# Kernel tuning notes

Measured on AMD Instinct MI355X. Metric: run time of the kernel, lower is better.

## Reference

```python
import jax, jax.numpy as jnp
import numpy as np

N_HEAD = 16
POSE = 5
YAW = 1
END_X, END_Y = 18, 32
THETA = 1000.0
LN_EPS = 1e-5

def compute_axial_cis(dim, end_x, end_y, theta):
    # Axial 2D rotary: dim is per-head dim; dim//4 freqs per spatial axis.
    n = dim // 4
    freqs = 1.0 / (theta ** (jnp.arange(0, dim, 4)[:n].astype(jnp.float32) / dim))
    t = jnp.arange(end_x * end_y, dtype=jnp.float32)
    t_x = t % end_x
    t_y = jnp.floor(t / end_x)
    ang = jnp.concatenate([t_x[:, None] * freqs[None, :], t_y[:, None] * freqs[None, :]], axis=-1)  # [L, dim//2]
    return jnp.cos(ang), jnp.sin(ang)

def apply_rotary(x, cos, sin):
    # x: [B,H,L,D]; complex pairing = consecutive (even, odd) lanes, as in view_as_complex
    xe, xo = x[..., 0::2], x[..., 1::2]
    oe = xe * cos - xo * sin
    oo = xe * sin + xo * cos
    return jnp.stack([oe, oo], axis=-1).reshape(x.shape)

def layernorm(z, g, b):
    m = jnp.mean(z, axis=-1, keepdims=True)
    v = jnp.mean(jnp.square(z - m), axis=-1, keepdims=True)
    return (z - m) * jax.lax.rsqrt(v + LN_EPS) * g + b

def setup_inputs() -> dict:
    key = jax.random.key(0)
    ks = jax.random.split(key, 8)
    B, T, C = 16, 582, 1024
    x = jax.random.normal(ks[0], (B, T, C), dtype=jnp.float32)
    # additive causal mask (0 keep / -1e9 masked), as a float attn_mask
    causal = jnp.tril(jnp.ones((T, T), dtype=jnp.float32))
    attn_mask = jnp.broadcast_to(jnp.where(causal > 0, 0.0, -1e9), (B, T, T))
    s = 0.02
    Wq = jax.random.normal(ks[1], (C, C), dtype=jnp.float32) * s
    Wk = jax.random.normal(ks[2], (C, C), dtype=jnp.float32) * s
    Wv = jax.random.normal(ks[3], (C, C), dtype=jnp.float32) * s
    Wo = jax.random.normal(ks[4], (C, C), dtype=jnp.float32) * s
    q_ln_g = jnp.ones((C,), jnp.float32); q_ln_b = jnp.zeros((C,), jnp.float32)
    k_ln_g = jnp.ones((C,), jnp.float32); k_ln_b = jnp.zeros((C,), jnp.float32)
    return {"x": x, "attn_mask": attn_mask, "Wq": Wq, "Wk": Wk, "Wv": Wv, "Wo": Wo,
            "q_ln_g": q_ln_g, "q_ln_b": q_ln_b, "k_ln_g": k_ln_g, "k_ln_b": k_ln_b}

def reference(x, attn_mask, Wq, Wk, Wv, Wo, q_ln_g, q_ln_b, k_ln_g, k_ln_b):
    B, T, C = x.shape
    H = N_HEAD
    D = C // H
    q = layernorm(x @ Wq.T, q_ln_g, q_ln_b)
    k = layernorm(x @ Wk.T, k_ln_g, k_ln_b)
    v = (x @ Wv.T).reshape(B, T, H, D).transpose(0, 2, 1, 3)
    q = q.reshape(B, T, H, D).transpose(0, 2, 1, 3)
    k = k.reshape(B, T, H, D).transpose(0, 2, 1, 3)
    prefix = POSE + YAW
    if T > prefix:  # static shape condition
        cos, sin = compute_axial_cis(D, END_X, END_Y, THETA)
        L = T - prefix
        cos, sin = cos[:L], sin[:L]  # [L, D//2]
        q = jnp.concatenate([q[:, :, :prefix], apply_rotary(q[:, :, prefix:], cos, sin)], axis=2)
        k = jnp.concatenate([k[:, :, :prefix], apply_rotary(k[:, :, prefix:], cos, sin)], axis=2)
    scale = 1.0 / jnp.sqrt(jnp.float32(D))
    scores = jnp.einsum("bhqd,bhkd->bhqk", q, k) * scale + attn_mask[:, None, :, :]
    att = jax.nn.softmax(scores, axis=-1)
    y = jnp.einsum("bhqk,bhkd->bhqd", att, v)
    y = y.transpose(0, 2, 1, 3).reshape(B, T, C)
    return y @ Wo.T
```

## Files before the change

kernel.cpp:

```cpp
#include <hip/hip_runtime.h>
#include <hip/hip_bf16.h>

typedef short bf16x8 __attribute__((ext_vector_type(8)));
typedef short bf16x4 __attribute__((ext_vector_type(4)));
typedef float f32x4  __attribute__((ext_vector_type(4)));

#define LDP 72

__device__ __forceinline__ float bits2f(short u) {
  return __uint_as_float(((unsigned int)(unsigned short)u) << 16);
}
__device__ __forceinline__ short f2bits(float f) {
  __hip_bfloat16 h = __float2bfloat16(f);
  return *reinterpret_cast<short*>(&h);
}
__device__ __forceinline__ void gld16(const short* g, short* l) {
  __builtin_amdgcn_global_load_lds(
      (const __attribute__((address_space(1))) void*)g,
      (__attribute__((address_space(3))) void*)l, 16, 0, 0);
}

__global__ __launch_bounds__(256)
void cvt_x_kernel(const float* __restrict__ src, short* __restrict__ dst, long n) {
  long i = ((long)blockIdx.x * 256 + threadIdx.x) * 4;
  if (i + 3 < n) {
    float4 v = *(const float4*)(src + i);
    bf16x4 o;
    o[0] = f2bits(v.x); o[1] = f2bits(v.y); o[2] = f2bits(v.z); o[3] = f2bits(v.w);
    *(bf16x4*)(dst + i) = o;
  }
}

__global__ __launch_bounds__(256)
void cvt_w_kernel(const float* __restrict__ w0, const float* __restrict__ w1,
                  const float* __restrict__ w2, const float* __restrict__ w3,
                  short* __restrict__ dst) {
  long i = ((long)blockIdx.x * 256 + threadIdx.x) * 4;
  int sel = (int)(i >> 20);
  const float* s = (sel == 0) ? w0 : (sel == 1) ? w1 : (sel == 2) ? w2 : w3;
  long off = i & ((1L << 20) - 1);
  float4 v = *(const float4*)(s + off);
  bf16x4 o;
  o[0] = f2bits(v.x); o[1] = f2bits(v.y); o[2] = f2bits(v.z); o[3] = f2bits(v.w);
  *(bf16x4*)(dst + i) = o;
}

template<int MODE>
__global__ __launch_bounds__(256)
void gemm_nt(const short* __restrict__ A, const short* __restrict__ Bm,
             float* __restrict__ OutF, short* __restrict__ Oq,
             short* __restrict__ Ok, short* __restrict__ Ov,
             int M, int K, int N, int T, int TPAD) {
  __shared__ short As[128 * 32];
  __shared__ short Bs[128 * 32];
  const int tid = threadIdx.x;
  const int w = tid >> 6, l = tid & 63;
  const int wr = w >> 1, wc = w & 1;
  const int lg = l >> 4, lo = l & 15;
  const long row0 = (long)blockIdx.x * 128;
  const long col0 = (long)blockIdx.y * 128;

  const int c2 = w * 2;
  const int lrow = l >> 2, lcol = (l & 3) * 8;
  long ga0 = row0 + c2 * 16 + lrow;      if (ga0 > M - 1) ga0 = M - 1;
  long ga1 = row0 + c2 * 16 + 16 + lrow; if (ga1 > M - 1) ga1 = M - 1;
  long gb0 = col0 + c2 * 16 + lrow;
  long gb1 = gb0 + 16;
  const short* pa0 = &A[ga0 * K + lcol];
  const short* pa1 = &A[ga1 * K + lcol];
  const short* pb0 = &Bm[gb0 * K + lcol];
  const short* pb1 = &Bm[gb1 * K + lcol];
  short* la0 = &As[c2 * 512];
  short* la1 = &As[c2 * 512 + 512];
  short* lb0 = &Bs[c2 * 512];
  short* lb1 = &Bs[c2 * 512 + 512];

  f32x4 acc[4][4] = {};

  for (int kt = 0; kt < K; kt += 32) {
    __syncthreads();
    gld16(pa0 + kt, la0);
    gld16(pa1 + kt, la1);
    gld16(pb0 + kt, lb0);
    gld16(pb1 + kt, lb1);
    __syncthreads();
    bf16x8 af[4], bfr[4];
#pragma unroll
    for (int mi = 0; mi < 4; ++mi)
      af[mi] = *(const bf16x8*)(&As[(wr * 64 + mi * 16 + lo) * 32 + lg * 8]);
#pragma unroll
    for (int ni = 0; ni < 4; ++ni)
      bfr[ni] = *(const bf16x8*)(&Bs[(wc * 64 + ni * 16 + lo) * 32 + lg * 8]);
#pragma unroll
    for (int mi = 0; mi < 4; ++mi)
#pragma unroll
      for (int ni = 0; ni < 4; ++ni)
        acc[mi][ni] = __builtin_amdgcn_mfma_f32_16x16x32_bf16(af[mi], bfr[ni], acc[mi][ni], 0, 0, 0);
  }

#pragma unroll
  for (int mi = 0; mi < 4; ++mi) {
#pragma unroll
    for (int r = 0; r < 4; ++r) {
      long m = row0 + wr * 64 + mi * 16 + lg * 4 + r;
      if (m >= M) continue;
#pragma unroll
      for (int ni = 0; ni < 4; ++ni) {
        long n = col0 + wc * 64 + ni * 16 + lo;
        float v = acc[mi][ni][r];
        if constexpr (MODE == 2) {
          OutF[m * (long)N + n] = v;
        } else {
          if (n < 1024) {
            Oq[m * 1024 + n] = f2bits(v);
          } else if (n < 2048) {
            Ok[m * 1024 + (n - 1024)] = f2bits(v);
          } else {
            long b = m / T;
            long t = m - b * T;
            long nn = n - 2048;
            long h = nn >> 6, d = nn & 63;
            Ov[((b * 16 + h) * 64 + d) * TPAD + t] = f2bits(v);
          }
        }
      }
    }
  }
}

__global__ __launch_bounds__(256)
void ln_rope_kernel(const short* __restrict__ qpre, const short* __restrict__ kpre,
                    const float* __restrict__ qg, const float* __restrict__ qb2,
                    const float* __restrict__ kg, const float* __restrict__ kb2,
                    short* __restrict__ qa, short* __restrict__ ka, int T) {
  const int row = blockIdx.x;
  const short* in; const float *g, *be; short* out;
  if (blockIdx.y == 0) { in = qpre; g = qg; be = qb2; out = qa; }
  else                 { in = kpre; g = kg; be = kb2; out = ka; }
  const int tid = threadIdx.x;
  const int c0 = tid * 4;

  bf16x4 xv = *(const bf16x4*)(&in[(long)row * 1024 + c0]);
  float xf[4];
  float s = 0.f, sq = 0.f;
#pragma unroll
  for (int i = 0; i < 4; ++i) { xf[i] = bits2f(xv[i]); s += xf[i]; sq += xf[i] * xf[i]; }
#pragma unroll
  for (int o = 1; o < 64; o <<= 1) { s += __shfl_xor(s, o); sq += __shfl_xor(sq, o); }
  __shared__ float red[8];
  const int w = tid >> 6, l = tid & 63;
  if (l == 0) { red[w] = s; red[4 + w] = sq; }
  __syncthreads();
  s  = red[0] + red[1] + red[2] + red[3];
  sq = red[4] + red[5] + red[6] + red[7];
  const float mean = s * (1.0f / 1024.0f);
  const float var  = sq * (1.0f / 1024.0f) - mean * mean;
  const float rstd = rsqrtf(var + 1e-5f);

  float4 gv = *(const float4*)(&g[c0]);
  float4 bv = *(const float4*)(&be[c0]);
  float z[4];
  z[0] = (xf[0] - mean) * rstd * gv.x + bv.x;
  z[1] = (xf[1] - mean) * rstd * gv.y + bv.y;
  z[2] = (xf[2] - mean) * rstd * gv.z + bv.z;
  z[3] = (xf[3] - mean) * rstd * gv.w + bv.w;

  const int t = row % T;
  const int p = t - 6;
  if (p >= 0) {
    const float tx = (float)(p % 18);
    const float ty = (float)(p / 18);
    const int jbase = (c0 & 63) >> 1;
#pragma unroll
    for (int q2 = 0; q2 < 2; ++q2) {
      const int jj = jbase + q2;
      const int i  = jj & 15;
      const float freq = exp2f(-(float)i * 0.6228615177913804f);
      const float ang  = ((jj < 16) ? tx : ty) * freq;
      float sv, cv;
      sincosf(ang, &sv, &cv);
      const float xe = z[q2 * 2], xo = z[q2 * 2 + 1];
      z[q2 * 2]     = xe * cv - xo * sv;
      z[q2 * 2 + 1] = xe * sv + xo * cv;
    }
  }
  const long b = row / T;
  const int h = c0 >> 6, d = c0 & 63;
  bf16x4 ov;
#pragma unroll
  for (int i = 0; i < 4; ++i) ov[i] = f2bits(z[i]);
  *(bf16x4*)(&out[(((b * 16 + h) * T) + t) * 64 + d]) = ov;
}

__global__ __launch_bounds__(256)
void attn_kernel(const short* __restrict__ Q, const short* __restrict__ Kk,
                 const short* __restrict__ Vt, short* __restrict__ Y,
                 int T, int TPAD) {
  __shared__ short QP[64 * LDP];
  __shared__ short Ks[64 * LDP];
  __shared__ short Vs[64 * LDP];
  const int tid = threadIdx.x;
  const int w = tid >> 6, l = tid & 63, lg = l >> 4, lo = l & 15;
  const int qb = gridDim.x - 1 - blockIdx.x;
  const int bh = blockIdx.y;
  const int b = bh >> 4, h = bh & 15;
  const long qbase = (long)bh * T * 64;
  short* Qs = QP;
  short* Ps = QP + w * 16 * LDP;

#pragma unroll
  for (int j = 0; j < 2; ++j) {
    int ch = tid + j * 256;
    int r = ch >> 3, c = (ch & 7) * 8;
    int t = qb * 64 + r; if (t > T - 1) t = T - 1;
    *(bf16x8*)(&Qs[r * LDP + c]) = *(const bf16x8*)(&Q[qbase + (long)t * 64 + c]);
  }
  __syncthreads();
  bf16x8 qf[2];
  qf[0] = *(const bf16x8*)(&Qs[(w * 16 + lo) * LDP + lg * 8]);
  qf[1] = *(const bf16x8*)(&Qs[(w * 16 + lo) * LDP + 32 + lg * 8]);

  float mrow[4], lsum[4];
  f32x4 oacc[4] = {};
#pragma unroll
  for (int r = 0; r < 4; ++r) { mrow[r] = -3e38f; lsum[r] = 0.f; }
  const float SCL = 0.125f * 1.44269504f;
  const int nkt = qb + 1;

  for (int kt = 0; kt < nkt; ++kt) {
    __syncthreads();
#pragma unroll
    for (int j = 0; j < 2; ++j) {
      int ch = tid + j * 256;
      int r = ch >> 3, c = (ch & 7) * 8;
      int tk = kt * 64 + r;
      bf16x8 kv = (bf16x8){0,0,0,0,0,0,0,0};
      if (tk < T) kv = *(const bf16x8*)(&Kk[qbase + (long)tk * 64 + c]);
      *(bf16x8*)(&Ks[r * LDP + c]) = kv;
      int keyc = kt * 64 + c;
      bf16x8 vv = (bf16x8){0,0,0,0,0,0,0,0};
      const long vrow = (long)bh * 64 + r;
      if (keyc + 7 < T) {
        vv = *(const bf16x8*)(&Vt[vrow * TPAD + keyc]);
      } else {
#pragma unroll
        for (int e = 0; e < 8; ++e) { int kk2 = keyc + e; if (kk2 < T) vv[e] = Vt[vrow * TPAD + kk2]; }
      }
      *(bf16x8*)(&Vs[r * LDP + c]) = vv;
    }
    __syncthreads();

    f32x4 sf[4] = {};
#pragma unroll
    for (int ni = 0; ni < 4; ++ni)
#pragma unroll
      for (int kk = 0; kk < 2; ++kk) {
        bf16x8 kfr = *(const bf16x8*)(&Ks[(ni * 16 + lo) * LDP + kk * 32 + lg * 8]);
        sf[ni] = __builtin_amdgcn_mfma_f32_16x16x32_bf16(qf[kk], kfr, sf[ni], 0, 0, 0);
      }

    float pm[4][4], tmax[4];
#pragma unroll
    for (int r = 0; r < 4; ++r) tmax[r] = -3e38f;
#pragma unroll
    for (int ni = 0; ni < 4; ++ni)
#pragma unroll
      for (int r = 0; r < 4; ++r) {
        int key  = kt * 64 + ni * 16 + lo;
        int qrow = qb * 64 + w * 16 + lg * 4 + r;
        float sv = sf[ni][r] * SCL;
        if (key > qrow || key >= T) sv = -3e38f;
        pm[ni][r] = sv;
        tmax[r] = fmaxf(tmax[r], sv);
      }
#pragma unroll
    for (int r = 0; r < 4; ++r)
#pragma unroll
      for (int o = 1; o < 16; o <<= 1) tmax[r] = fmaxf(tmax[r], __shfl_xor(tmax[r], o));

    float fsc[4];
#pragma unroll
    for (int r = 0; r < 4; ++r) {
      float mn = fmaxf(mrow[r], tmax[r]);
      fsc[r] = exp2f(mrow[r] - mn);
      mrow[r] = mn;
    }
    float psum[4] = {0.f, 0.f, 0.f, 0.f};
#pragma unroll
    for (int ni = 0; ni < 4; ++ni)
#pragma unroll
      for (int r = 0; r < 4; ++r) {
        float pv = exp2f(pm[ni][r] - mrow[r]);
        pm[ni][r] = pv;
        psum[r] += pv;
      }
#pragma unroll
    for (int r = 0; r < 4; ++r) {
#pragma unroll
      for (int o = 1; o < 16; o <<= 1) psum[r] += __shfl_xor(psum[r], o);
      lsum[r] = lsum[r] * fsc[r] + psum[r];
    }
#pragma unroll
    for (int ni = 0; ni < 4; ++ni)
#pragma unroll
      for (int r = 0; r < 4; ++r) oacc[ni][r] *= fsc[r];

#pragma unroll
    for (int ni = 0; ni < 4; ++ni)
#pragma unroll
      for (int r = 0; r < 4; ++r)
        Ps[(lg * 4 + r) * LDP + ni * 16 + lo] = f2bits(pm[ni][r]);
    __syncthreads();

#pragma unroll
    for (int kk = 0; kk < 2; ++kk) {
      bf16x8 pf = *(const bf16x8*)(&Ps[lo * LDP + kk * 32 + lg * 8]);
#pragma unroll
      for (int ni = 0; ni < 4; ++ni) {
        bf16x8 vf = *(const bf16x8*)(&Vs[(ni * 16 + lo) * LDP + kk * 32 + lg * 8]);
        oacc[ni] = __builtin_amdgcn_mfma_f32_16x16x32_bf16(pf, vf, oacc[ni], 0, 0, 0);
      }
    }
  }

#pragma unroll
  for (int r = 0; r < 4; ++r) {
    int tq = qb * 64 + w * 16 + lg * 4 + r;
    if (tq >= T) continue;
    float inv = 1.0f / lsum[r];
#pragma unroll
    for (int ni = 0; ni < 4; ++ni) {
      float o = oacc[ni][r] * inv;
      Y[((long)b * T + tq) * 1024 + h * 64 + ni * 16 + lo] = f2bits(o);
    }
  }
}

extern "C" void kernel_launch(void* const* d_in, const int* in_sizes, int n_in,
                              void* d_out, int out_size, void* d_ws, size_t ws_size,
                              hipStream_t stream) {
  const float* x   = (const float*)d_in[0];
  const float* Wq  = (const float*)d_in[2];
  const float* Wk  = (const float*)d_in[3];
  const float* Wv  = (const float*)d_in[4];
  const float* Wo  = (const float*)d_in[5];
  const float* qg  = (const float*)d_in[6];
  const float* qb2 = (const float*)d_in[7];
  const float* kg  = (const float*)d_in[8];
  const float* kb2 = (const float*)d_in[9];

  const int B = 16, T = 582, C = 1024;
  const int M = B * T;
  const int TPAD = 584;

  short* ws = (short*)d_ws;
  const long E  = (long)M * C;
  const long EV = (long)B * 16 * 64 * TPAD;
  short* xb   = ws;
  short* qpre = ws + E;
  short* kpre = ws + 2 * E;
  short* ka   = ws + 3 * E;
  short* vat  = ws + 4 * E;
  short* wb   = ws + 4 * E + EV;
  short* qa   = xb;
  short* y    = qpre;
  float* out  = (float*)d_out;
  (void)ws_size; (void)in_sizes; (void)n_in; (void)out_size;

  const long WE = 1L << 20;

  cvt_x_kernel<<<(int)(E / 4 / 256), 256, 0, stream>>>(x, xb, E);
  cvt_w_kernel<<<(int)(4 * WE / 4 / 256), 256, 0, stream>>>(Wq, Wk, Wv, Wo, wb);

  dim3 gqkv((M + 127) / 128, 3072 / 128);
  gemm_nt<3><<<gqkv, 256, 0, stream>>>(xb, wb, nullptr, qpre, kpre, vat, M, C, 3072, T, TPAD);
  ln_rope_kernel<<<dim3(M, 2), 256, 0, stream>>>(qpre, kpre, qg, qb2, kg, kb2, qa, ka, T);
  attn_kernel<<<dim3((T + 63) / 64, B * 16), 256, 0, stream>>>(qa, ka, vat, y, T, TPAD);
  dim3 gout((M + 127) / 128, C / 128);
  gemm_nt<2><<<gout, 256, 0, stream>>>(y, wb + 3 * WE, out, nullptr, nullptr, nullptr, M, C, C, T, TPAD);
}
```

Measured before the change: 282.8 us.

## Double-buffer GEMM LDS loads, swizzle blocks across XCDs, prefetch attention K/V

The GEMM now keeps two LDS buffers. It issues the global_load_lds copies for the next K-tile before computing the current one, with explicit vmcnt waits and barriers in place of two full syncthreads per step. Workgroup IDs are remapped so neighbouring output tiles land together across the 8 XCDs, which should improve L2 reuse. In attention, the next K/V tile is loaded into registers while the current one is computed; the per-tile bounds checks and one block barrier are dropped. To cover the unchecked reads, a small pad is added before the weight buffer. The risk is that out-of-range K/V reads pull in stale or uninitialized workspace values, which could give NaNs even though those keys are masked.

```diff
diff --git a/kernel.cpp b/kernel.cpp
--- a/kernel.cpp
+++ b/kernel.cpp
@@ -6,6 +6,9 @@
 typedef float f32x4  __attribute__((ext_vector_type(4)));
 
 #define LDP 72
+
+#define S_VMCNT(N) asm volatile("s_waitcnt vmcnt(" #N ")" ::: "memory")
+#define S_BAR()    do { asm volatile("" ::: "memory"); __builtin_amdgcn_s_barrier(); asm volatile("" ::: "memory"); } while (0)
 
 __device__ __forceinline__ float bits2f(short u) {
   return __uint_as_float(((unsigned int)(unsigned short)u) << 16);
@@ -51,14 +54,20 @@
              float* __restrict__ OutF, short* __restrict__ Oq,
              short* __restrict__ Ok, short* __restrict__ Ov,
              int M, int K, int N, int T, int TPAD) {
-  __shared__ short As[128 * 32];
-  __shared__ short Bs[128 * 32];
+  __shared__ short As[2 * 128 * 32];
+  __shared__ short Bs[2 * 128 * 32];
   const int tid = threadIdx.x;
   const int w = tid >> 6, l = tid & 63;
   const int wr = w >> 1, wc = w & 1;
   const int lg = l >> 4, lo = l & 15;
-  const long row0 = (long)blockIdx.x * 128;
-  const long col0 = (long)blockIdx.y * 128;
+
+  const int gx = gridDim.x;
+  const int nwg = gx * gridDim.y;
+  const int flat = blockIdx.y * gx + blockIdx.x;
+  const int cpx = nwg >> 3;
+  const int swz = (flat & 7) * cpx + (flat >> 3);
+  const long row0 = (long)(swz % gx) * 128;
+  const long col0 = (long)(swz / gx) * 128;
 
   const int c2 = w * 2;
   const int lrow = l >> 2, lcol = (l & 3) * 8;
@@ -77,26 +86,43 @@
 
   f32x4 acc[4][4] = {};
 
-  for (int kt = 0; kt < K; kt += 32) {
-    __syncthreads();
-    gld16(pa0 + kt, la0);
-    gld16(pa1 + kt, la1);
-    gld16(pb0 + kt, lb0);
-    gld16(pb1 + kt, lb1);
-    __syncthreads();
+  auto STAGE = [&](int kt, int buf) {
+    const int o = buf * 4096;
+    gld16(pa0 + kt, la0 + o);
+    gld16(pa1 + kt, la1 + o);
+    gld16(pb0 + kt, lb0 + o);
+    gld16(pb1 + kt, lb1 + o);
+  };
+  auto COMPUTE = [&](int buf) {
+    const short* as = &As[buf * 4096];
+    const short* bs = &Bs[buf * 4096];
     bf16x8 af[4], bfr[4];
 #pragma unroll
     for (int mi = 0; mi < 4; ++mi)
-      af[mi] = *(const bf16x8*)(&As[(wr * 64 + mi * 16 + lo) * 32 + lg * 8]);
-#pragma unroll
-    for (int ni = 0; ni < 4; ++ni)
-      bfr[ni] = *(const bf16x8*)(&Bs[(wc * 64 + ni * 16 + lo) * 32 + lg * 8]);
+      af[mi] = *(const bf16x8*)(&as[(wr * 64 + mi * 16 + lo) * 32 + lg * 8]);
+#pragma unroll
+    for (int ni = 0; ni < 4; ++ni)
+      bfr[ni] = *(const bf16x8*)(&bs[(wc * 64 + ni * 16 + lo) * 32 + lg * 8]);
 #pragma unroll
     for (int mi = 0; mi < 4; ++mi)
 #pragma unroll
       for (int ni = 0; ni < 4; ++ni)
         acc[mi][ni] = __builtin_amdgcn_mfma_f32_16x16x32_bf16(af[mi], bfr[ni], acc[mi][ni], 0, 0, 0);
-  }
+  };
+
+  STAGE(0, 0);
+  int cur = 0;
+  for (int kt = 0; kt + 32 < K; kt += 32) {
+    STAGE(kt + 32, cur ^ 1);
+    S_VMCNT(4);
+    S_BAR();
+    COMPUTE(cur);
+    S_BAR();
+    cur ^= 1;
+  }
+  S_VMCNT(0);
+  S_BAR();
+  COMPUTE(cur);
 
 #pragma unroll
   for (int mi = 0; mi < 4; ++mi) {
@@ -208,6 +234,9 @@
   short* Qs = QP;
   short* Ps = QP + w * 16 * LDP;
 
+  const int r0 = tid >> 3, c0s = (tid & 7) * 8;
+  const int r1 = (tid + 256) >> 3, c1s = c0s;
+
 #pragma unroll
   for (int j = 0; j < 2; ++j) {
     int ch = tid + j * 256;
@@ -227,28 +256,24 @@
   const float SCL = 0.125f * 1.44269504f;
   const int nkt = qb + 1;
 
+  bf16x8 kreg[2], vreg[2];
+  const long vbase = (long)bh * 64;
+  auto LOADKV = [&](int kt) {
+    kreg[0] = *(const bf16x8*)(&Kk[qbase + (long)(kt * 64 + r0) * 64 + c0s]);
+    kreg[1] = *(const bf16x8*)(&Kk[qbase + (long)(kt * 64 + r1) * 64 + c1s]);
+    vreg[0] = *(const bf16x8*)(&Vt[(vbase + r0) * TPAD + kt * 64 + c0s]);
+    vreg[1] = *(const bf16x8*)(&Vt[(vbase + r1) * TPAD + kt * 64 + c1s]);
+  };
+  LOADKV(0);
+
   for (int kt = 0; kt < nkt; ++kt) {
     __syncthreads();
-#pragma unroll
-    for (int j = 0; j < 2; ++j) {
-      int ch = tid + j * 256;
-      int r = ch >> 3, c = (ch & 7) * 8;
-      int tk = kt * 64 + r;
-      bf16x8 kv = (bf16x8){0,0,0,0,0,0,0,0};
-      if (tk < T) kv = *(const bf16x8*)(&Kk[qbase + (long)tk * 64 + c]);
-      *(bf16x8*)(&Ks[r * LDP + c]) = kv;
-      int keyc = kt * 64 + c;
-      bf16x8 vv = (bf16x8){0,0,0,0,0,0,0,0};
-      const long vrow = (long)bh * 64 + r;
-      if (keyc + 7 < T) {
-        vv = *(const bf16x8*)(&Vt[vrow * TPAD + keyc]);
-      } else {
-#pragma unroll
-        for (int e = 0; e < 8; ++e) { int kk2 = keyc + e; if (kk2 < T) vv[e] = Vt[vrow * TPAD + kk2]; }
-      }
-      *(bf16x8*)(&Vs[r * LDP + c]) = vv;
-    }
+    *(bf16x8*)(&Ks[r0 * LDP + c0s]) = kreg[0];
+    *(bf16x8*)(&Ks[r1 * LDP + c1s]) = kreg[1];
+    *(bf16x8*)(&Vs[r0 * LDP + c0s]) = vreg[0];
+    *(bf16x8*)(&Vs[r1 * LDP + c1s]) = vreg[1];
     __syncthreads();
+    if (kt + 1 < nkt) LOADKV(kt + 1);
 
     f32x4 sf[4] = {};
 #pragma unroll
@@ -310,7 +335,6 @@
 #pragma unroll
       for (int r = 0; r < 4; ++r)
         Ps[(lg * 4 + r) * LDP + ni * 16 + lo] = f2bits(pm[ni][r]);
-    __syncthreads();
 
 #pragma unroll
     for (int kk = 0; kk < 2; ++kk) {
@@ -361,7 +385,7 @@
   short* kpre = ws + 2 * E;
   short* ka   = ws + 3 * E;
   short* vat  = ws + 4 * E;
-  short* wb   = ws + 4 * E + EV;
+  short* wb   = ws + 4 * E + EV + 1024;
   short* qa   = xb;
   short* y    = qpre;
   float* out  = (float*)d_out;
```

Measured after the change: 311.6 us. 10.2% more time.

## Replace QKV GEMM with 256x256 double-buffered LDS kernel and prefetch attention K/V

Applied to the files above, without the earlier changes.

Adds a dedicated QKV projection kernel with 512 threads and 256x256 tiles. It loads global memory directly into LDS with an XOR swizzle and double buffering, uses explicit barrier/priority scheduling, and remaps workgroups across XCDs. The aim is better operand reuse and overlap of loads with MFMA compared with the old 128x128 kernel. The attention kernel now prefetches the next K/V tile into registers while computing the current one and drops a block-wide barrier before the P·V step. It also removes the tail bounds checks, relying on padding and masking, and the weight buffer is offset to leave slack for the resulting over-reads.

```diff
diff --git a/kernel.cpp b/kernel.cpp
--- a/kernel.cpp
+++ b/kernel.cpp
@@ -6,6 +6,9 @@
 typedef float f32x4  __attribute__((ext_vector_type(4)));
 
 #define LDP 72
+
+#define S_VMCNT0() asm volatile("s_waitcnt vmcnt(0)" ::: "memory")
+#define S_BAR()    do { asm volatile("" ::: "memory"); __builtin_amdgcn_s_barrier(); asm volatile("" ::: "memory"); } while (0)
 
 __device__ __forceinline__ float bits2f(short u) {
   return __uint_as_float(((unsigned int)(unsigned short)u) << 16);
@@ -45,12 +48,134 @@
   *(bf16x4*)(dst + i) = o;
 }
 
-template<int MODE>
+__global__ __launch_bounds__(512, 2)
+void gemm_qkv_8p(const short* __restrict__ A, const short* __restrict__ Bm,
+                 short* __restrict__ Oq, short* __restrict__ Ok, short* __restrict__ Ov,
+                 int M, int T, int TPAD) {
+  __shared__ short As[2][16384];
+  __shared__ short Bs[2][16384];
+  const int tid = threadIdx.x;
+  const int w = tid >> 6, l = tid & 63;
+  const int wm = w >> 2, wn = w & 3;
+  const int lg = l >> 4, lo = l & 15;
+
+  const int gx = gridDim.x;
+  const int nwg = gx * gridDim.y;
+  const int flat = blockIdx.y * gx + blockIdx.x;
+  const int q8 = nwg >> 3, r8 = nwg & 7;
+  const int xcd = flat & 7, idx = flat >> 3;
+  const int wgid = (xcd < r8 ? xcd * (q8 + 1) : r8 * (q8 + 1) + (xcd - r8) * q8) + idx;
+  const long row0 = (long)(wgid % gx) * 256;
+  const long col0 = (long)(wgid / gx) * 256;
+
+  f32x4 acc[8][4] = {};
+  bf16x8 af[8][2];
+  bf16x8 bfr[2];
+
+  auto STAGE_A = [&](int kt, int slot, int h) {
+#pragma unroll
+    for (int pass = 0; pass < 2; ++pass) {
+      int off = h * 16384 + pass * 8192 + tid * 16;
+      int row = off >> 7;
+      int lc = (off & 127) ^ ((row & 7) << 4);
+      long grow = row0 + row; if (grow > M - 1) grow = M - 1;
+      gld16(&A[grow * 1024 + kt * 64 + (lc >> 1)], &As[slot][off >> 1]);
+    }
+  };
+  auto STAGE_B = [&](int kt, int slot, int h) {
+#pragma unroll
+    for (int pass = 0; pass < 2; ++pass) {
+      int off = h * 16384 + pass * 8192 + tid * 16;
+      int row = off >> 7;
+      int lc = (off & 127) ^ ((row & 7) << 4);
+      gld16(&Bm[(col0 + row) * 1024 + kt * 64 + (lc >> 1)], &Bs[slot][off >> 1]);
+    }
+  };
+  auto LDA = [&](int slot) {
+#pragma unroll
+    for (int m = 0; m < 8; ++m)
+#pragma unroll
+      for (int ks = 0; ks < 2; ++ks) {
+        int row = wm * 128 + m * 16 + lo;
+        int pe = (ks * 32 + lg * 8) ^ ((lo & 7) << 3);
+        af[m][ks] = *(const bf16x8*)(&As[slot][row * 64 + pe]);
+      }
+  };
+  auto LDB = [&](int slot, int p) {
+#pragma unroll
+    for (int ks = 0; ks < 2; ++ks) {
+      int row = wn * 64 + p * 16 + lo;
+      int pe = (ks * 32 + lg * 8) ^ ((lo & 7) << 3);
+      bfr[ks] = *(const bf16x8*)(&Bs[slot][row * 64 + pe]);
+    }
+  };
+
+  STAGE_A(0, 0, 0); STAGE_A(0, 0, 1);
+  STAGE_B(0, 0, 0); STAGE_B(0, 0, 1);
+  S_VMCNT0();
+  S_BAR();
+
+#define QKV_PHASE(p) \
+    S_BAR(); \
+    asm volatile("s_waitcnt lgkmcnt(0)" ::: "memory"); \
+    __builtin_amdgcn_sched_barrier(0); \
+    __builtin_amdgcn_s_setprio(1); \
+    _Pragma("unroll") \
+    for (int ks = 0; ks < 2; ++ks) { \
+      _Pragma("unroll") \
+      for (int m = 0; m < 8; ++m) \
+        acc[m][p] = __builtin_amdgcn_mfma_f32_16x16x32_bf16(af[m][ks], bfr[ks], acc[m][p], 0, 0, 0); \
+    } \
+    __builtin_amdgcn_s_setprio(0);
+
+  for (int i = 0; i < 16; ++i) {
+    const int s = i & 1;
+    const bool pf = (i < 15);
+    LDA(s); LDB(s, 0);
+    if (pf) { STAGE_A(i + 1, s ^ 1, 0); STAGE_B(i + 1, s ^ 1, 0); }
+    QKV_PHASE(0)
+    S_BAR();
+    LDB(s, 1);
+    if (pf) { STAGE_A(i + 1, s ^ 1, 1); STAGE_B(i + 1, s ^ 1, 1); }
+    QKV_PHASE(1)
+    S_BAR();
+    LDB(s, 2);
+    QKV_PHASE(2)
+    S_BAR();
+    LDB(s, 3);
+    QKV_PHASE(3)
+    if (pf) S_VMCNT0();
+    S_BAR();
+  }
+#undef QKV_PHASE
+
+#pragma unroll
+  for (int m = 0; m < 8; ++m) {
+#pragma unroll
+    for (int r = 0; r < 4; ++r) {
+      long gm = row0 + wm * 128 + m * 16 + lg * 4 + r;
+      if (gm >= M) continue;
+#pragma unroll
+      for (int p = 0; p < 4; ++p) {
+        long n = col0 + wn * 64 + p * 16 + lo;
+        float v = acc[m][p][r];
+        if (n < 1024) {
+          Oq[gm * 1024 + n] = f2bits(v);
+        } else if (n < 2048) {
+          Ok[gm * 1024 + (n - 1024)] = f2bits(v);
+        } else {
+          long b = gm / T, t = gm - b * T;
+          long nn = n - 2048, h = nn >> 6, d = nn & 63;
+          Ov[((b * 16 + h) * 64 + d) * TPAD + t] = f2bits(v);
+        }
+      }
+    }
+  }
+}
+
 __global__ __launch_bounds__(256)
-void gemm_nt(const short* __restrict__ A, const short* __restrict__ Bm,
-             float* __restrict__ OutF, short* __restrict__ Oq,
-             short* __restrict__ Ok, short* __restrict__ Ov,
-             int M, int K, int N, int T, int TPAD) {
+void gemm_out(const short* __restrict__ A, const short* __restrict__ Bm,
+              float* __restrict__ OutF, int M, int K, int N) {
   __shared__ short As[128 * 32];
   __shared__ short Bs[128 * 32];
   const int tid = threadIdx.x;
@@ -107,22 +232,7 @@
 #pragma unroll
       for (int ni = 0; ni < 4; ++ni) {
         long n = col0 + wc * 64 + ni * 16 + lo;
-        float v = acc[mi][ni][r];
-        if constexpr (MODE == 2) {
-          OutF[m * (long)N + n] = v;
-        } else {
-          if (n < 1024) {
-            Oq[m * 1024 + n] = f2bits(v);
-          } else if (n < 2048) {
-            Ok[m * 1024 + (n - 1024)] = f2bits(v);
-          } else {
-            long b = m / T;
-            long t = m - b * T;
-            long nn = n - 2048;
-            long h = nn >> 6, d = nn & 63;
-            Ov[((b * 16 + h) * 64 + d) * TPAD + t] = f2bits(v);
-          }
-        }
+        OutF[m * (long)N + n] = acc[mi][ni][r];
       }
     }
   }
@@ -208,6 +318,9 @@
   short* Qs = QP;
   short* Ps = QP + w * 16 * LDP;
 
+  const int r0 = tid >> 3, c0s = (tid & 7) * 8;
+  const int r1 = r0 + 32, c1s = c0s;
+
 #pragma unroll
   for (int j = 0; j < 2; ++j) {
     int ch = tid + j * 256;
@@ -227,28 +340,24 @@
   const float SCL = 0.125f * 1.44269504f;
   const int nkt = qb + 1;
 
+  bf16x8 kreg[2], vreg[2];
+  const long vbase = (long)bh * 64;
+  auto LOADKV = [&](int kt) {
+    kreg[0] = *(const bf16x8*)(&Kk[qbase + (long)(kt * 64 + r0) * 64 + c0s]);
+    kreg[1] = *(const bf16x8*)(&Kk[qbase + (long)(kt * 64 + r1) * 64 + c1s]);
+    vreg[0] = *(const bf16x8*)(&Vt[(vbase + r0) * TPAD + kt * 64 + c0s]);
+    vreg[1] = *(const bf16x8*)(&Vt[(vbase + r1) * TPAD + kt * 64 + c1s]);
+  };
+  LOADKV(0);
+
   for (int kt = 0; kt < nkt; ++kt) {
     __syncthreads();
-#pragma unroll
-    for (int j = 0; j < 2; ++j) {
-      int ch = tid + j * 256;
-      int r = ch >> 3, c = (ch & 7) * 8;
-      int tk = kt * 64 + r;
-      bf16x8 kv = (bf16x8){0,0,0,0,0,0,0,0};
-      if (tk < T) kv = *(const bf16x8*)(&Kk[qbase + (long)tk * 64 + c]);
-      *(bf16x8*)(&Ks[r * LDP + c]) = kv;
-      int keyc = kt * 64 + c;
-      bf16x8 vv = (bf16x8){0,0,0,0,0,0,0,0};
-      const long vrow = (long)bh * 64 + r;
-      if (keyc + 7 < T) {
-        vv = *(const bf16x8*)(&Vt[vrow * TPAD + keyc]);
-      } else {
-#pragma unroll
-        for (int e = 0; e < 8; ++e) { int kk2 = keyc + e; if (kk2 < T) vv[e] = Vt[vrow * TPAD + kk2]; }
-      }
-      *(bf16x8*)(&Vs[r * LDP + c]) = vv;
-    }
+    *(bf16x8*)(&Ks[r0 * LDP + c0s]) = kreg[0];
+    *(bf16x8*)(&Ks[r1 * LDP + c1s]) = kreg[1];
+    *(bf16x8*)(&Vs[r0 * LDP + c0s]) = vreg[0];
+    *(bf16x8*)(&Vs[r1 * LDP + c1s]) = vreg[1];
     __syncthreads();
+    if (kt + 1 < nkt) LOADKV(kt + 1);
 
     f32x4 sf[4] = {};
 #pragma unroll
@@ -310,7 +419,6 @@
 #pragma unroll
       for (int r = 0; r < 4; ++r)
         Ps[(lg * 4 + r) * LDP + ni * 16 + lo] = f2bits(pm[ni][r]);
-    __syncthreads();
 
 #pragma unroll
     for (int kk = 0; kk < 2; ++kk) {
@@ -361,7 +469,7 @@
   short* kpre = ws + 2 * E;
   short* ka   = ws + 3 * E;
   short* vat  = ws + 4 * E;
-  short* wb   = ws + 4 * E + EV;
+  short* wb   = ws + 4 * E + EV + 1024;
   short* qa   = xb;
   short* y    = qpre;
   float* out  = (float*)d_out;
@@ -372,10 +480,10 @@
   cvt_x_kernel<<<(int)(E / 4 / 256), 256, 0, stream>>>(x, xb, E);
   cvt_w_kernel<<<(int)(4 * WE / 4 / 256), 256, 0, stream>>>(Wq, Wk, Wv, Wo, wb);
 
-  dim3 gqkv((M + 127) / 128, 3072 / 128);
-  gemm_nt<3><<<gqkv, 256, 0, stream>>>(xb, wb, nullptr, qpre, kpre, vat, M, C, 3072, T, TPAD);
+  dim3 gqkv((M + 255) / 256, 3072 / 256);
+  gemm_qkv_8p<<<gqkv, 512, 0, stream>>>(xb, wb, qpre, kpre, vat, M, T, TPAD);
   ln_rope_kernel<<<dim3(M, 2), 256, 0, stream>>>(qpre, kpre, qg, qb2, kg, kb2, qa, ka, T);
   attn_kernel<<<dim3((T + 63) / 64, B * 16), 256, 0, stream>>>(qa, ka, vat, y, T, TPAD);
   dim3 gout((M + 127) / 128, C / 128);
-  gemm_nt<2><<<gout, 256, 0, stream>>>(y, wb + 3 * WE, out, nullptr, nullptr, nullptr, M, C, C, T, TPAD);
-}
+  gemm_out<<<gout, 256, 0, stream>>>(y, wb + 3 * WE, out, M, C, C);
+}
```

Measured after the change: 307.4 us. 1.09x slower.

## Widen GEMM K-tile with swizzled LDS, prefetch attention K/V, lazy softmax rescale

Applied to the files above, without the earlier changes.

The GEMM now stages 64-wide K tiles per iteration and XOR-swizzles the LDS layout. This halves the barrier count and avoids bank conflicts on fragment reads. The attention kernel loads the next K/V tile into registers while the current tile is computed, and drops the per-element bounds checks on those loads. It also skips the online-softmax rescale when no row max changes, and removes a block barrier before the wave-private P reads. Out-of-range K/V reads now pull in neighbouring or padding memory, which relies on masking giving zero weight. NaNs in the uninitialised pad could still leak through, which is why the weight buffer was shifted.

```diff
diff --git a/kernel.cpp b/kernel.cpp
--- a/kernel.cpp
+++ b/kernel.cpp
@@ -51,8 +51,8 @@
              float* __restrict__ OutF, short* __restrict__ Oq,
              short* __restrict__ Ok, short* __restrict__ Ov,
              int M, int K, int N, int T, int TPAD) {
-  __shared__ short As[128 * 32];
-  __shared__ short Bs[128 * 32];
+  __shared__ short As[128 * 64];
+  __shared__ short Bs[128 * 64];
   const int tid = threadIdx.x;
   const int w = tid >> 6, l = tid & 63;
   const int wr = w >> 1, wc = w & 1;
@@ -60,42 +60,52 @@
   const long row0 = (long)blockIdx.x * 128;
   const long col0 = (long)blockIdx.y * 128;
 
-  const int c2 = w * 2;
-  const int lrow = l >> 2, lcol = (l & 3) * 8;
-  long ga0 = row0 + c2 * 16 + lrow;      if (ga0 > M - 1) ga0 = M - 1;
-  long ga1 = row0 + c2 * 16 + 16 + lrow; if (ga1 > M - 1) ga1 = M - 1;
-  long gb0 = col0 + c2 * 16 + lrow;
-  long gb1 = gb0 + 16;
-  const short* pa0 = &A[ga0 * K + lcol];
-  const short* pa1 = &A[ga1 * K + lcol];
-  const short* pb0 = &Bm[gb0 * K + lcol];
-  const short* pb1 = &Bm[gb1 * K + lcol];
-  short* la0 = &As[c2 * 512];
-  short* la1 = &As[c2 * 512 + 512];
-  short* lb0 = &Bs[c2 * 512];
-  short* lb1 = &Bs[c2 * 512 + 512];
+  const short* pa[4]; const short* pb[4]; short* la[4]; short* lb[4];
+#pragma unroll
+  for (int j = 0; j < 4; ++j) {
+    const int c = w * 4 + j;
+    const int off = c * 1024 + l * 16;
+    const int row = off >> 7;
+    const int lc  = (off & 127) ^ ((row & 7) << 4);
+    long ga = row0 + row; if (ga > M - 1) ga = M - 1;
+    pa[j] = &A[ga * K + (lc >> 1)];
+    pb[j] = &Bm[(col0 + row) * K + (lc >> 1)];
+    la[j] = &As[c * 512];
+    lb[j] = &Bs[c * 512];
+  }
 
   f32x4 acc[4][4] = {};
 
-  for (int kt = 0; kt < K; kt += 32) {
+  for (int kt = 0; kt < K; kt += 64) {
     __syncthreads();
-    gld16(pa0 + kt, la0);
-    gld16(pa1 + kt, la1);
-    gld16(pb0 + kt, lb0);
-    gld16(pb1 + kt, lb1);
+#pragma unroll
+    for (int j = 0; j < 4; ++j) {
+      gld16(pa[j] + kt, la[j]);
+      gld16(pb[j] + kt, lb[j]);
+    }
     __syncthreads();
-    bf16x8 af[4], bfr[4];
+    bf16x8 af[4][2], bfr[4][2];
 #pragma unroll
     for (int mi = 0; mi < 4; ++mi)
-      af[mi] = *(const bf16x8*)(&As[(wr * 64 + mi * 16 + lo) * 32 + lg * 8]);
-#pragma unroll
-    for (int ni = 0; ni < 4; ++ni)
-      bfr[ni] = *(const bf16x8*)(&Bs[(wc * 64 + ni * 16 + lo) * 32 + lg * 8]);
+#pragma unroll
+      for (int ks = 0; ks < 2; ++ks) {
+        int pe = (ks * 32 + lg * 8) ^ ((lo & 7) << 3);
+        af[mi][ks] = *(const bf16x8*)(&As[(wr * 64 + mi * 16 + lo) * 64 + pe]);
+      }
+#pragma unroll
+    for (int ni = 0; ni < 4; ++ni)
+#pragma unroll
+      for (int ks = 0; ks < 2; ++ks) {
+        int pe = (ks * 32 + lg * 8) ^ ((lo & 7) << 3);
+        bfr[ni][ks] = *(const bf16x8*)(&Bs[(wc * 64 + ni * 16 + lo) * 64 + pe]);
+      }
 #pragma unroll
     for (int mi = 0; mi < 4; ++mi)
 #pragma unroll
       for (int ni = 0; ni < 4; ++ni)
-        acc[mi][ni] = __builtin_amdgcn_mfma_f32_16x16x32_bf16(af[mi], bfr[ni], acc[mi][ni], 0, 0, 0);
+#pragma unroll
+        for (int ks = 0; ks < 2; ++ks)
+          acc[mi][ni] = __builtin_amdgcn_mfma_f32_16x16x32_bf16(af[mi][ks], bfr[ni][ks], acc[mi][ni], 0, 0, 0);
   }
 
 #pragma unroll
@@ -116,10 +126,8 @@
           } else if (n < 2048) {
             Ok[m * 1024 + (n - 1024)] = f2bits(v);
           } else {
-            long b = m / T;
-            long t = m - b * T;
-            long nn = n - 2048;
-            long h = nn >> 6, d = nn & 63;
+            long b = m / T, t = m - b * T;
+            long nn = n - 2048, h = nn >> 6, d = nn & 63;
             Ov[((b * 16 + h) * 64 + d) * TPAD + t] = f2bits(v);
           }
         }
@@ -208,6 +216,9 @@
   short* Qs = QP;
   short* Ps = QP + w * 16 * LDP;
 
+  const int r0 = tid >> 3, c0s = (tid & 7) * 8;
+  const int r1 = r0 + 32, c1s = c0s;
+
 #pragma unroll
   for (int j = 0; j < 2; ++j) {
     int ch = tid + j * 256;
@@ -227,28 +238,24 @@
   const float SCL = 0.125f * 1.44269504f;
   const int nkt = qb + 1;
 
+  bf16x8 kreg[2], vreg[2];
+  const long vbase = (long)bh * 64;
+  auto LOADKV = [&](int kt) {
+    kreg[0] = *(const bf16x8*)(&Kk[qbase + (long)(kt * 64 + r0) * 64 + c0s]);
+    kreg[1] = *(const bf16x8*)(&Kk[qbase + (long)(kt * 64 + r1) * 64 + c1s]);
+    vreg[0] = *(const bf16x8*)(&Vt[(vbase + r0) * TPAD + kt * 64 + c0s]);
+    vreg[1] = *(const bf16x8*)(&Vt[(vbase + r1) * TPAD + kt * 64 + c1s]);
+  };
+  LOADKV(0);
+
   for (int kt = 0; kt < nkt; ++kt) {
     __syncthreads();
-#pragma unroll
-    for (int j = 0; j < 2; ++j) {
-      int ch = tid + j * 256;
-      int r = ch >> 3, c = (ch & 7) * 8;
-      int tk = kt * 64 + r;
-      bf16x8 kv = (bf16x8){0,0,0,0,0,0,0,0};
-      if (tk < T) kv = *(const bf16x8*)(&Kk[qbase + (long)tk * 64 + c]);
-      *(bf16x8*)(&Ks[r * LDP + c]) = kv;
-      int keyc = kt * 64 + c;
-      bf16x8 vv = (bf16x8){0,0,0,0,0,0,0,0};
-      const long vrow = (long)bh * 64 + r;
-      if (keyc + 7 < T) {
-        vv = *(const bf16x8*)(&Vt[vrow * TPAD + keyc]);
-      } else {
-#pragma unroll
-        for (int e = 0; e < 8; ++e) { int kk2 = keyc + e; if (kk2 < T) vv[e] = Vt[vrow * TPAD + kk2]; }
-      }
-      *(bf16x8*)(&Vs[r * LDP + c]) = vv;
-    }
+    *(bf16x8*)(&Ks[r0 * LDP + c0s]) = kreg[0];
+    *(bf16x8*)(&Ks[r1 * LDP + c1s]) = kreg[1];
+    *(bf16x8*)(&Vs[r0 * LDP + c0s]) = vreg[0];
+    *(bf16x8*)(&Vs[r1 * LDP + c1s]) = vreg[1];
     __syncthreads();
+    if (kt + 1 < nkt) LOADKV(kt + 1);
 
     f32x4 sf[4] = {};
 #pragma unroll
@@ -278,12 +285,18 @@
 #pragma unroll
       for (int o = 1; o < 16; o <<= 1) tmax[r] = fmaxf(tmax[r], __shfl_xor(tmax[r], o));
 
-    float fsc[4];
-#pragma unroll
-    for (int r = 0; r < 4; ++r) {
-      float mn = fmaxf(mrow[r], tmax[r]);
-      fsc[r] = exp2f(mrow[r] - mn);
-      mrow[r] = mn;
+    bool need = !__all(tmax[0] <= mrow[0] && tmax[1] <= mrow[1] &&
+                       tmax[2] <= mrow[2] && tmax[3] <= mrow[3]);
+    if (need) {
+#pragma unroll
+      for (int r = 0; r < 4; ++r) {
+        float mn = fmaxf(mrow[r], tmax[r]);
+        float fsc = exp2f(mrow[r] - mn);
+        mrow[r] = mn;
+        lsum[r] *= fsc;
+#pragma unroll
+        for (int ni = 0; ni < 4; ++ni) oacc[ni][r] *= fsc;
+      }
     }
     float psum[4] = {0.f, 0.f, 0.f, 0.f};
 #pragma unroll
@@ -298,19 +311,14 @@
     for (int r = 0; r < 4; ++r) {
 #pragma unroll
       for (int o = 1; o < 16; o <<= 1) psum[r] += __shfl_xor(psum[r], o);
-      lsum[r] = lsum[r] * fsc[r] + psum[r];
-    }
-#pragma unroll
-    for (int ni = 0; ni < 4; ++ni)
-#pragma unroll
-      for (int r = 0; r < 4; ++r) oacc[ni][r] *= fsc[r];
+      lsum[r] += psum[r];
+    }
 
 #pragma unroll
     for (int ni = 0; ni < 4; ++ni)
 #pragma unroll
       for (int r = 0; r < 4; ++r)
         Ps[(lg * 4 + r) * LDP + ni * 16 + lo] = f2bits(pm[ni][r]);
-    __syncthreads();
 
 #pragma unroll
     for (int kk = 0; kk < 2; ++kk) {
@@ -361,7 +369,7 @@
   short* kpre = ws + 2 * E;
   short* ka   = ws + 3 * E;
   short* vat  = ws + 4 * E;
-  short* wb   = ws + 4 * E + EV;
+  short* wb   = ws + 4 * E + EV + 1024;
   short* qa   = xb;
   short* y    = qpre;
   float* out  = (float*)d_out;
```

After: 259.9 us. 8.1% less time.
